# Performance work log

Measured on AMD Instinct MI355X. Metric: run time of the kernel, lower is better.

Reference implementation:

```python
import jax, jax.numpy as jnp
import numpy as np

N_NODES = 100000


def setup_inputs() -> dict:
    key = jax.random.key(0)
    k1, k2, k3, k4, k5 = jax.random.split(key, 5)
    h = jax.random.normal(k1, (N_NODES, 128), dtype=jnp.float32)
    norm = jax.random.uniform(k2, (N_NODES, 1), dtype=jnp.float32)  # D^{-1/2}-style per-node norm
    W = jax.random.normal(k3, (128, 64), dtype=jnp.float32) * 0.05
    b = jnp.zeros((64,), dtype=jnp.float32)
    src = jax.random.randint(k4, (1600000,), 0, N_NODES, dtype=jnp.int32)
    dst = jax.random.randint(k5, (1600000,), 0, N_NODES, dtype=jnp.int32)
    return {"h": h, "norm": norm, "W": W, "b": b, "src": src, "dst": dst}


def reference(h, norm, W, b, src, dst):
    # Dense feature transform: g.ndata['h'] = h @ W   (dropout is identity at inference)
    hw = jnp.matmul(h, W)  # [N, out]
    # Message: src feature scaled by src norm
    msg = hw[src] * norm[src]  # [E, out]
    # Reduce: sum messages into dst, scale by dst norm
    agg = jax.ops.segment_sum(msg, dst, num_segments=N_NODES) * norm  # [N, out]
    out = agg + b
    return jax.nn.relu(out)
```

## Files before the change

kernel.cpp:

```cpp
#include <hip/hip_runtime.h>


typedef unsigned int u32;
typedef unsigned short u16;
typedef __attribute__((ext_vector_type(8))) short s16x8;
typedef __attribute__((ext_vector_type(4))) float f32x4;

#define NB_LOG 6
#define NPB 64
#define CAP 2048
#define MAXB 2048
#define EPB 8192
#define RT 256

__device__ __forceinline__ float bf2f(u16 v) {
  return __uint_as_float(((u32)v) << 16);
}
__device__ __forceinline__ u16 f2bf(float f) {
  u32 u = __float_as_uint(f);
  return (u16)((u + 0x7fffu + ((u >> 16) & 1u)) >> 16);
}

__global__ __launch_bounds__(256) void wconv(
    const float* __restrict__ W, u16* __restrict__ Wtg, u32* __restrict__ gcur) {
  int o = blockIdx.x * 256 + threadIdx.x;
  int j = o & 7, col = (o >> 3) & 15, kq = (o >> 7) & 3, ks = (o >> 9) & 3,
      ct = (o >> 11) & 3;
  int k = ks * 32 + kq * 8 + j;
  int n = ct * 16 + col;
  Wtg[o] = f2bf(W[k * 64 + n]);
  if (o < MAXB) gcur[o] = 0;
}

__global__ __launch_bounds__(256) void gemm_mfma(
    const float* __restrict__ h, const float* __restrict__ norm,
    const u16* __restrict__ Wtg, u16* __restrict__ scaledh, int N) {
  int lane = threadIdx.x & 63, wid = threadIdx.x >> 6;
  int col = lane & 15, kq = lane >> 4;

  s16x8 bfrag[4][4];
#pragma unroll
  for (int ct = 0; ct < 4; ++ct)
#pragma unroll
    for (int ks = 0; ks < 4; ++ks) {
      int f = ct * 16 + ks * 4 + kq;
      bfrag[ct][ks] = *reinterpret_cast<const s16x8*>(Wtg + ((size_t)(f * 16 + col) * 8));
    }

  int row0 = blockIdx.x * 64 + wid * 16;
  int myrow = row0 + col;
  int ldrow = myrow < N ? myrow : (N - 1);
  const float* __restrict__ hrow = h + (size_t)ldrow * 128 + kq * 8;

  f32x4 acc[4];
#pragma unroll
  for (int ct = 0; ct < 4; ++ct) acc[ct] = (f32x4){0.f, 0.f, 0.f, 0.f};

#pragma unroll
  for (int ks = 0; ks < 4; ++ks) {
    float4 x0 = *reinterpret_cast<const float4*>(hrow + ks * 32);
    float4 x1 = *reinterpret_cast<const float4*>(hrow + ks * 32 + 4);
    s16x8 a;
    a[0] = (short)f2bf(x0.x); a[1] = (short)f2bf(x0.y);
    a[2] = (short)f2bf(x0.z); a[3] = (short)f2bf(x0.w);
    a[4] = (short)f2bf(x1.x); a[5] = (short)f2bf(x1.y);
    a[6] = (short)f2bf(x1.z); a[7] = (short)f2bf(x1.w);
#pragma unroll
    for (int ct = 0; ct < 4; ++ct)
      acc[ct] = __builtin_amdgcn_mfma_f32_16x16x32_bf16(a, bfrag[ct][ks], acc[ct], 0, 0, 0);
  }

#pragma unroll
  for (int reg = 0; reg < 4; ++reg) {
    int node = row0 + kq * 4 + reg;
    if (node < N) {
      float nm = norm[node];
#pragma unroll
      for (int ct = 0; ct < 4; ++ct)
        scaledh[(size_t)node * 64 + ct * 16 + col] = f2bf(acc[ct][reg] * nm);
    }
  }
}

__global__ __launch_bounds__(1024) void bin_edges(
    const int* __restrict__ src, const int* __restrict__ dst,
    u32* __restrict__ gcur, u32* __restrict__ bins, int E) {
  __shared__ u32 lhist[MAXB];
  __shared__ u32 lbase[MAXB];
  int t = threadIdx.x;
  for (int i = t; i < MAXB; i += 1024) lhist[i] = 0;
  __syncthreads();
  int e0 = blockIdx.x * EPB;
  int s[8], d[8];
  u32 r[8];
#pragma unroll
  for (int k = 0; k < 8; ++k) {
    int e = e0 + k * 1024 + t;
    bool ok = e < E;
    s[k] = ok ? src[e] : 0;
    d[k] = ok ? dst[e] : -1;
  }
#pragma unroll
  for (int k = 0; k < 8; ++k) {
    if (d[k] >= 0) r[k] = atomicAdd(&lhist[d[k] >> NB_LOG], 1u);
  }
  __syncthreads();
  for (int i = t; i < MAXB; i += 1024) {
    u32 c = lhist[i];
    lbase[i] = c ? atomicAdd(&gcur[i], c) : 0u;
  }
  __syncthreads();
#pragma unroll
  for (int k = 0; k < 8; ++k) {
    if (d[k] >= 0) {
      int bk = d[k] >> NB_LOG;
      u32 p = lbase[bk] + r[k];
      if (p < CAP)
        bins[(size_t)bk * CAP + p] = ((u32)s[k] << NB_LOG) | (u32)(d[k] & (NPB - 1));
    }
  }
}

__global__ __launch_bounds__(RT) void bucket_reduce(
    const u16* __restrict__ scaledh, const u32* __restrict__ bins,
    const u32* __restrict__ gcur, const float* __restrict__ norm,
    const float4* __restrict__ bias4, float* __restrict__ out, int N) {
  __shared__ u32 hist[NPB];
  __shared__ u32 startp[NPB + 1];
  __shared__ u32 sorted[CAP];
  int bkt = blockIdx.x;
  int t = threadIdx.x, lane = t & 63, wid = t >> 6;
  int cnt = (int)gcur[bkt];
  if (cnt > CAP) cnt = CAP;
  if (t < NPB) hist[t] = 0;
  __syncthreads();

  const u32* __restrict__ my = bins + (size_t)bkt * CAP;
  u32 w[CAP / RT];
  u32 rk[CAP / RT];
#pragma unroll
  for (int k = 0; k < CAP / RT; ++k) {
    int e = k * RT + t;
    w[k] = (e < cnt) ? my[e] : 0xFFFFFFFFu;
  }
#pragma unroll
  for (int k = 0; k < CAP / RT; ++k) {
    if (w[k] != 0xFFFFFFFFu)
      rk[k] = atomicAdd(&hist[w[k] & (NPB - 1)], 1u);
  }
  __syncthreads();
  if (t < NPB) {
    u32 v = hist[t];
    u32 inc = v;
#pragma unroll
    for (int m = 1; m < NPB; m <<= 1) {
      u32 x = __shfl_up(inc, m);
      if (t >= m) inc += x;
    }
    startp[t] = inc - v;
    if (t == NPB - 1) startp[NPB] = inc;
  }
  __syncthreads();
#pragma unroll
  for (int k = 0; k < CAP / RT; ++k) {
    if (w[k] != 0xFFFFFFFFu)
      sorted[startp[w[k] & (NPB - 1)] + rk[k]] = w[k] >> NB_LOG;
  }
  __syncthreads();

  int grp = lane >> 4, c4 = lane & 15;
  float4 bl = bias4[c4];
  int base = bkt << NB_LOG;
  for (int rr = wid; rr < NPB; rr += 8) {
    int rA = rr, rB = rr + 4;
    int nodeA = base + rA, nodeB = base + rB;
    int jA = (int)startp[rA] + grp, endA = (int)startp[rA + 1];
    int jB = (int)startp[rB] + grp, endB = (int)startp[rB + 1];
    float4 aA = make_float4(0.f, 0.f, 0.f, 0.f);
    float4 aB = make_float4(0.f, 0.f, 0.f, 0.f);
    while (jA < endA || jB < endB) {
      if (jA < endA) {
        int s = (int)sorted[jA];
        uint2 v = *reinterpret_cast<const uint2*>(scaledh + (size_t)s * 64 + c4 * 4);
        aA.x += __uint_as_float(v.x << 16);
        aA.y += __uint_as_float(v.x & 0xFFFF0000u);
        aA.z += __uint_as_float(v.y << 16);
        aA.w += __uint_as_float(v.y & 0xFFFF0000u);
        jA += 4;
      }
      if (jB < endB) {
        int s = (int)sorted[jB];
        uint2 v = *reinterpret_cast<const uint2*>(scaledh + (size_t)s * 64 + c4 * 4);
        aB.x += __uint_as_float(v.x << 16);
        aB.y += __uint_as_float(v.x & 0xFFFF0000u);
        aB.z += __uint_as_float(v.y << 16);
        aB.w += __uint_as_float(v.y & 0xFFFF0000u);
        jB += 4;
      }
    }
#pragma unroll
    for (int m = 16; m <= 32; m <<= 1) {
      aA.x += __shfl_xor(aA.x, m); aA.y += __shfl_xor(aA.y, m);
      aA.z += __shfl_xor(aA.z, m); aA.w += __shfl_xor(aA.w, m);
      aB.x += __shfl_xor(aB.x, m); aB.y += __shfl_xor(aB.y, m);
      aB.z += __shfl_xor(aB.z, m); aB.w += __shfl_xor(aB.w, m);
    }
    if (grp == 0) {
      if (nodeA < N) {
        float nm = norm[nodeA];
        float4 o;
        o.x = fmaxf(fmaf(aA.x, nm, bl.x), 0.f);
        o.y = fmaxf(fmaf(aA.y, nm, bl.y), 0.f);
        o.z = fmaxf(fmaf(aA.z, nm, bl.z), 0.f);
        o.w = fmaxf(fmaf(aA.w, nm, bl.w), 0.f);
        *reinterpret_cast<float4*>(out + (size_t)nodeA * 64 + c4 * 4) = o;
      }
      if (nodeB < N) {
        float nm = norm[nodeB];
        float4 o;
        o.x = fmaxf(fmaf(aB.x, nm, bl.x), 0.f);
        o.y = fmaxf(fmaf(aB.y, nm, bl.y), 0.f);
        o.z = fmaxf(fmaf(aB.z, nm, bl.z), 0.f);
        o.w = fmaxf(fmaf(aB.w, nm, bl.w), 0.f);
        *reinterpret_cast<float4*>(out + (size_t)nodeB * 64 + c4 * 4) = o;
      }
    }
  }
}

__global__ __launch_bounds__(256) void zero_out(float4* __restrict__ o4, size_t n4) {
  size_t tid = blockIdx.x * 256 + threadIdx.x;
  size_t stride = (size_t)gridDim.x * 256;
  for (size_t i = tid; i < n4; i += stride) o4[i] = make_float4(0.f, 0.f, 0.f, 0.f);
}

__global__ __launch_bounds__(256) void scatter_edges(
    const u16* __restrict__ scaledh, const int* __restrict__ src,
    const int* __restrict__ dst, float* __restrict__ agg, int E) {
  int lane = threadIdx.x & 63;
  int gwid = (blockIdx.x * 256 + threadIdx.x) >> 6;
  int nw = (gridDim.x * 256) >> 6;
  for (int e = gwid; e < E; e += nw) {
    int s = __builtin_amdgcn_readfirstlane(src[e]);
    int d = __builtin_amdgcn_readfirstlane(dst[e]);
    float v = bf2f(scaledh[(size_t)s * 64 + lane]);
    unsafeAtomicAdd(&agg[(size_t)d * 64 + lane], v);
  }
}

__global__ __launch_bounds__(256) void finalize(
    float4* __restrict__ out4, const float* __restrict__ norm,
    const float4* __restrict__ b4, int N) {
  size_t total4 = (size_t)N * 16;
  size_t tid = blockIdx.x * 256 + threadIdx.x;
  size_t stride = (size_t)gridDim.x * 256;
  for (size_t t = tid; t < total4; t += stride) {
    int i = (int)(t >> 4), q = (int)(t & 15);
    float4 v = out4[t];
    float nm = norm[i];
    float4 bb = b4[q];
    v.x = fmaxf(fmaf(v.x, nm, bb.x), 0.f);
    v.y = fmaxf(fmaf(v.y, nm, bb.y), 0.f);
    v.z = fmaxf(fmaf(v.z, nm, bb.z), 0.f);
    v.w = fmaxf(fmaf(v.w, nm, bb.w), 0.f);
    out4[t] = v;
  }
}

extern "C" void kernel_launch(void* const* d_in, const int* in_sizes, int n_in,
                              void* d_out, int out_size, void* d_ws, size_t ws_size,
                              hipStream_t stream) {
  const float* h    = (const float*)d_in[0];
  const float* norm = (const float*)d_in[1];
  const float* W    = (const float*)d_in[2];
  const float* b    = (const float*)d_in[3];
  const int*   src  = (const int*)d_in[4];
  const int*   dst  = (const int*)d_in[5];

  int N = in_sizes[1];
  int E = in_sizes[4];
  int nbuckets = (N + NPB - 1) >> NB_LOG;
  int nrb = (N + 63) >> 6;

  char* ws = (char*)d_ws;
  size_t off = 0;
  u16* scaledh = (u16*)(ws + off); off += (((size_t)N * 64 * 2) + 255) & ~(size_t)255;
  u32* gcur    = (u32*)(ws + off); off += (MAXB * 4 + 255) & ~(size_t)255;
  u16* Wtg     = (u16*)(ws + off); off += (8192 * 2 + 255) & ~(size_t)255;
  u32* bins    = (u32*)(ws + off); off += (size_t)MAXB * CAP * 4;
  size_t needed = off;
  size_t needed_fb = (size_t)((char*)bins - ws);

  if (ws_size >= needed && nbuckets <= MAXB) {
    wconv<<<32, 256, 0, stream>>>(W, Wtg, gcur);
    gemm_mfma<<<nrb, 256, 0, stream>>>(h, norm, Wtg, scaledh, N);
    bin_edges<<<(E + EPB - 1) / EPB, 1024, 0, stream>>>(src, dst, gcur, bins, E);
    bucket_reduce<<<nbuckets, RT, 0, stream>>>(scaledh, bins, gcur, norm,
                                               (const float4*)b, (float*)d_out, N);
  } else if (ws_size >= needed_fb) {
    float* agg = (float*)d_out;
    wconv<<<32, 256, 0, stream>>>(W, Wtg, gcur);
    gemm_mfma<<<nrb, 256, 0, stream>>>(h, norm, Wtg, scaledh, N);
    zero_out<<<1024, 256, 0, stream>>>((float4*)agg, (size_t)N * 16);
    scatter_edges<<<2048, 256, 0, stream>>>(scaledh, src, dst, agg, E);
    finalize<<<1024, 256, 0, stream>>>((float4*)agg, norm, (const float4*)b, N);
  }
}
```

Before: 88.28 us.

## Fuse GEMM and edge binning into one launch; restructure bucket reduce gather

```diff
diff --git a/kernel.cpp b/kernel.cpp
--- a/kernel.cpp
+++ b/kernel.cpp
@@ -19,6 +19,12 @@
 __device__ __forceinline__ u16 f2bf(float f) {
   u32 u = __float_as_uint(f);
   return (u16)((u + 0x7fffu + ((u >> 16) & 1u)) >> 16);
+}
+__device__ __forceinline__ void acc_bf16x4(float4& a, uint2 v) {
+  a.x += __uint_as_float(v.x << 16);
+  a.y += __uint_as_float(v.x & 0xFFFF0000u);
+  a.z += __uint_as_float(v.y << 16);
+  a.w += __uint_as_float(v.y & 0xFFFF0000u);
 }
 
 __global__ __launch_bounds__(256) void wconv(
@@ -32,91 +38,92 @@
   if (o < MAXB) gcur[o] = 0;
 }
 
-__global__ __launch_bounds__(256) void gemm_mfma(
+__global__ __launch_bounds__(256) void gemm_and_bin(
     const float* __restrict__ h, const float* __restrict__ norm,
-    const u16* __restrict__ Wtg, u16* __restrict__ scaledh, int N) {
-  int lane = threadIdx.x & 63, wid = threadIdx.x >> 6;
-  int col = lane & 15, kq = lane >> 4;
-
-  s16x8 bfrag[4][4];
-#pragma unroll
-  for (int ct = 0; ct < 4; ++ct)
-#pragma unroll
-    for (int ks = 0; ks < 4; ++ks) {
-      int f = ct * 16 + ks * 4 + kq;
-      bfrag[ct][ks] = *reinterpret_cast<const s16x8*>(Wtg + ((size_t)(f * 16 + col) * 8));
-    }
-
-  int row0 = blockIdx.x * 64 + wid * 16;
-  int myrow = row0 + col;
-  int ldrow = myrow < N ? myrow : (N - 1);
-  const float* __restrict__ hrow = h + (size_t)ldrow * 128 + kq * 8;
-
-  f32x4 acc[4];
-#pragma unroll
-  for (int ct = 0; ct < 4; ++ct) acc[ct] = (f32x4){0.f, 0.f, 0.f, 0.f};
-
-#pragma unroll
-  for (int ks = 0; ks < 4; ++ks) {
-    float4 x0 = *reinterpret_cast<const float4*>(hrow + ks * 32);
-    float4 x1 = *reinterpret_cast<const float4*>(hrow + ks * 32 + 4);
-    s16x8 a;
-    a[0] = (short)f2bf(x0.x); a[1] = (short)f2bf(x0.y);
-    a[2] = (short)f2bf(x0.z); a[3] = (short)f2bf(x0.w);
-    a[4] = (short)f2bf(x1.x); a[5] = (short)f2bf(x1.y);
-    a[6] = (short)f2bf(x1.z); a[7] = (short)f2bf(x1.w);
-#pragma unroll
-    for (int ct = 0; ct < 4; ++ct)
-      acc[ct] = __builtin_amdgcn_mfma_f32_16x16x32_bf16(a, bfrag[ct][ks], acc[ct], 0, 0, 0);
-  }
-
-#pragma unroll
-  for (int reg = 0; reg < 4; ++reg) {
-    int node = row0 + kq * 4 + reg;
-    if (node < N) {
-      float nm = norm[node];
-#pragma unroll
-      for (int ct = 0; ct < 4; ++ct)
-        scaledh[(size_t)node * 64 + ct * 16 + col] = f2bf(acc[ct][reg] * nm);
-    }
-  }
-}
-
-__global__ __launch_bounds__(1024) void bin_edges(
+    const u16* __restrict__ Wtg, u16* __restrict__ scaledh, int N, int nrb,
     const int* __restrict__ src, const int* __restrict__ dst,
     u32* __restrict__ gcur, u32* __restrict__ bins, int E) {
-  __shared__ u32 lhist[MAXB];
+  __shared__ u32 hist[MAXB];
   __shared__ u32 lbase[MAXB];
+
+  if ((int)blockIdx.x < nrb) {
+    int lane = threadIdx.x & 63, wid = threadIdx.x >> 6;
+    int col = lane & 15, kq = lane >> 4;
+
+    s16x8 bfrag[4][4];
+#pragma unroll
+    for (int ct = 0; ct < 4; ++ct)
+#pragma unroll
+      for (int ks = 0; ks < 4; ++ks) {
+        int f = ct * 16 + ks * 4 + kq;
+        bfrag[ct][ks] =
+            *reinterpret_cast<const s16x8*>(Wtg + ((size_t)(f * 16 + col) * 8));
+      }
+
+    int row0 = blockIdx.x * 64 + wid * 16;
+    int myrow = row0 + col;
+    int ldrow = myrow < N ? myrow : (N - 1);
+    const float* __restrict__ hrow = h + (size_t)ldrow * 128 + kq * 8;
+
+    f32x4 acc[4];
+#pragma unroll
+    for (int ct = 0; ct < 4; ++ct) acc[ct] = (f32x4){0.f, 0.f, 0.f, 0.f};
+
+#pragma unroll
+    for (int ks = 0; ks < 4; ++ks) {
+      float4 x0 = *reinterpret_cast<const float4*>(hrow + ks * 32);
+      float4 x1 = *reinterpret_cast<const float4*>(hrow + ks * 32 + 4);
+      s16x8 a;
+      a[0] = (short)f2bf(x0.x); a[1] = (short)f2bf(x0.y);
+      a[2] = (short)f2bf(x0.z); a[3] = (short)f2bf(x0.w);
+      a[4] = (short)f2bf(x1.x); a[5] = (short)f2bf(x1.y);
+      a[6] = (short)f2bf(x1.z); a[7] = (short)f2bf(x1.w);
+#pragma unroll
+      for (int ct = 0; ct < 4; ++ct)
+        acc[ct] =
+            __builtin_amdgcn_mfma_f32_16x16x32_bf16(a, bfrag[ct][ks], acc[ct], 0, 0, 0);
+    }
+
+#pragma unroll
+    for (int reg = 0; reg < 4; ++reg) {
+      int node = row0 + kq * 4 + reg;
+      if (node < N) {
+        float nm = norm[node];
+#pragma unroll
+        for (int ct = 0; ct < 4; ++ct)
+          scaledh[(size_t)node * 64 + ct * 16 + col] = f2bf(acc[ct][reg] * nm);
+      }
+    }
+    return;
+  }
+
+  int bid = (int)blockIdx.x - nrb;
   int t = threadIdx.x;
-  for (int i = t; i < MAXB; i += 1024) lhist[i] = 0;
-  __syncthreads();
-  int e0 = blockIdx.x * EPB;
-  int s[8], d[8];
-  u32 r[8];
-#pragma unroll
-  for (int k = 0; k < 8; ++k) {
-    int e = e0 + k * 1024 + t;
-    bool ok = e < E;
-    s[k] = ok ? src[e] : 0;
-    d[k] = ok ? dst[e] : -1;
-  }
-#pragma unroll
-  for (int k = 0; k < 8; ++k) {
-    if (d[k] >= 0) r[k] = atomicAdd(&lhist[d[k] >> NB_LOG], 1u);
-  }
-  __syncthreads();
-  for (int i = t; i < MAXB; i += 1024) {
-    u32 c = lhist[i];
+  for (int i = t; i < MAXB; i += 256) hist[i] = 0;
+  __syncthreads();
+  int e0 = bid * EPB;
+#pragma unroll 4
+  for (int k = 0; k < EPB / 256; ++k) {
+    int e = e0 + k * 256 + t;
+    if (e < E) atomicAdd(&hist[dst[e] >> NB_LOG], 1u);
+  }
+  __syncthreads();
+  for (int i = t; i < MAXB; i += 256) {
+    u32 c = hist[i];
     lbase[i] = c ? atomicAdd(&gcur[i], c) : 0u;
   }
   __syncthreads();
-#pragma unroll
-  for (int k = 0; k < 8; ++k) {
-    if (d[k] >= 0) {
-      int bk = d[k] >> NB_LOG;
-      u32 p = lbase[bk] + r[k];
+  for (int i = t; i < MAXB; i += 256) hist[i] = 0;
+  __syncthreads();
+#pragma unroll 4
+  for (int k = 0; k < EPB / 256; ++k) {
+    int e = e0 + k * 256 + t;
+    if (e < E) {
+      int d = dst[e], s = src[e];
+      int bk = d >> NB_LOG;
+      u32 p = lbase[bk] + atomicAdd(&hist[bk], 1u);
       if (p < CAP)
-        bins[(size_t)bk * CAP + p] = ((u32)s[k] << NB_LOG) | (u32)(d[k] & (NPB - 1));
+        bins[(size_t)bk * CAP + p] = ((u32)s << NB_LOG) | (u32)(d & (NPB - 1));
     }
   }
 }
@@ -171,59 +178,54 @@
   int grp = lane >> 4, c4 = lane & 15;
   float4 bl = bias4[c4];
   int base = bkt << NB_LOG;
-  for (int rr = wid; rr < NPB; rr += 8) {
-    int rA = rr, rB = rr + 4;
-    int nodeA = base + rA, nodeB = base + rB;
-    int jA = (int)startp[rA] + grp, endA = (int)startp[rA + 1];
-    int jB = (int)startp[rB] + grp, endB = (int)startp[rB + 1];
+  int cm1 = cnt - 1;
+#pragma unroll
+  for (int round = 0; round < 2; ++round) {
+    int rA = (wid << 4) + (round << 3) + grp;
+    int rB = rA + 4;
+    int jA = (int)startp[rA], eA = (int)startp[rA + 1];
+    int jB = (int)startp[rB], eB = (int)startp[rB + 1];
     float4 aA = make_float4(0.f, 0.f, 0.f, 0.f);
     float4 aB = make_float4(0.f, 0.f, 0.f, 0.f);
-    while (jA < endA || jB < endB) {
-      if (jA < endA) {
-        int s = (int)sorted[jA];
-        uint2 v = *reinterpret_cast<const uint2*>(scaledh + (size_t)s * 64 + c4 * 4);
-        aA.x += __uint_as_float(v.x << 16);
-        aA.y += __uint_as_float(v.x & 0xFFFF0000u);
-        aA.z += __uint_as_float(v.y << 16);
-        aA.w += __uint_as_float(v.y & 0xFFFF0000u);
-        jA += 4;
-      }
-      if (jB < endB) {
-        int s = (int)sorted[jB];
-        uint2 v = *reinterpret_cast<const uint2*>(scaledh + (size_t)s * 64 + c4 * 4);
-        aB.x += __uint_as_float(v.x << 16);
-        aB.y += __uint_as_float(v.x & 0xFFFF0000u);
-        aB.z += __uint_as_float(v.y << 16);
-        aB.w += __uint_as_float(v.y & 0xFFFF0000u);
-        jB += 4;
-      }
-    }
-#pragma unroll
-    for (int m = 16; m <= 32; m <<= 1) {
-      aA.x += __shfl_xor(aA.x, m); aA.y += __shfl_xor(aA.y, m);
-      aA.z += __shfl_xor(aA.z, m); aA.w += __shfl_xor(aA.w, m);
-      aB.x += __shfl_xor(aB.x, m); aB.y += __shfl_xor(aB.y, m);
-      aB.z += __shfl_xor(aB.z, m); aB.w += __shfl_xor(aB.w, m);
-    }
-    if (grp == 0) {
-      if (nodeA < N) {
-        float nm = norm[nodeA];
-        float4 o;
-        o.x = fmaxf(fmaf(aA.x, nm, bl.x), 0.f);
-        o.y = fmaxf(fmaf(aA.y, nm, bl.y), 0.f);
-        o.z = fmaxf(fmaf(aA.z, nm, bl.z), 0.f);
-        o.w = fmaxf(fmaf(aA.w, nm, bl.w), 0.f);
-        *reinterpret_cast<float4*>(out + (size_t)nodeA * 64 + c4 * 4) = o;
-      }
-      if (nodeB < N) {
-        float nm = norm[nodeB];
-        float4 o;
-        o.x = fmaxf(fmaf(aB.x, nm, bl.x), 0.f);
-        o.y = fmaxf(fmaf(aB.y, nm, bl.y), 0.f);
-        o.z = fmaxf(fmaf(aB.z, nm, bl.z), 0.f);
-        o.w = fmaxf(fmaf(aB.w, nm, bl.w), 0.f);
-        *reinterpret_cast<float4*>(out + (size_t)nodeB * 64 + c4 * 4) = o;
-      }
+    while (jA < eA || jB < eB) {
+      int iA0 = (int)sorted[min(jA, cm1)];
+      int iA1 = (int)sorted[min(jA + 1, cm1)];
+      int iB0 = (int)sorted[min(jB, cm1)];
+      int iB1 = (int)sorted[min(jB + 1, cm1)];
+      uint2 vA0 = *reinterpret_cast<const uint2*>(scaledh + ((size_t)iA0 << 6) + (c4 << 2));
+      uint2 vA1 = *reinterpret_cast<const uint2*>(scaledh + ((size_t)iA1 << 6) + (c4 << 2));
+      uint2 vB0 = *reinterpret_cast<const uint2*>(scaledh + ((size_t)iB0 << 6) + (c4 << 2));
+      uint2 vB1 = *reinterpret_cast<const uint2*>(scaledh + ((size_t)iB1 << 6) + (c4 << 2));
+      uint2 z = make_uint2(0u, 0u);
+      vA0 = (jA < eA) ? vA0 : z;
+      vA1 = (jA + 1 < eA) ? vA1 : z;
+      vB0 = (jB < eB) ? vB0 : z;
+      vB1 = (jB + 1 < eB) ? vB1 : z;
+      acc_bf16x4(aA, vA0);
+      acc_bf16x4(aA, vA1);
+      acc_bf16x4(aB, vB0);
+      acc_bf16x4(aB, vB1);
+      jA += 2;
+      jB += 2;
+    }
+    int nodeA = base + rA, nodeB = base + rB;
+    if (nodeA < N) {
+      float nm = norm[nodeA];
+      float4 o;
+      o.x = fmaxf(fmaf(aA.x, nm, bl.x), 0.f);
+      o.y = fmaxf(fmaf(aA.y, nm, bl.y), 0.f);
+      o.z = fmaxf(fmaf(aA.z, nm, bl.z), 0.f);
+      o.w = fmaxf(fmaf(aA.w, nm, bl.w), 0.f);
+      *reinterpret_cast<float4*>(out + (size_t)nodeA * 64 + (c4 << 2)) = o;
+    }
+    if (nodeB < N) {
+      float nm = norm[nodeB];
+      float4 o;
+      o.x = fmaxf(fmaf(aB.x, nm, bl.x), 0.f);
+      o.y = fmaxf(fmaf(aB.y, nm, bl.y), 0.f);
+      o.z = fmaxf(fmaf(aB.z, nm, bl.z), 0.f);
+      o.w = fmaxf(fmaf(aB.w, nm, bl.w), 0.f);
+      *reinterpret_cast<float4*>(out + (size_t)nodeB * 64 + (c4 << 2)) = o;
     }
   }
 }
@@ -281,6 +283,7 @@
   int E = in_sizes[4];
   int nbuckets = (N + NPB - 1) >> NB_LOG;
   int nrb = (N + 63) >> 6;
+  int nbinb = (E + EPB - 1) / EPB;
 
   char* ws = (char*)d_ws;
   size_t off = 0;
@@ -293,14 +296,15 @@
 
   if (ws_size >= needed && nbuckets <= MAXB) {
     wconv<<<32, 256, 0, stream>>>(W, Wtg, gcur);
-    gemm_mfma<<<nrb, 256, 0, stream>>>(h, norm, Wtg, scaledh, N);
-    bin_edges<<<(E + EPB - 1) / EPB, 1024, 0, stream>>>(src, dst, gcur, bins, E);
+    gemm_and_bin<<<nrb + nbinb, 256, 0, stream>>>(h, norm, Wtg, scaledh, N, nrb,
+                                                  src, dst, gcur, bins, E);
     bucket_reduce<<<nbuckets, RT, 0, stream>>>(scaledh, bins, gcur, norm,
                                                (const float4*)b, (float*)d_out, N);
   } else if (ws_size >= needed_fb) {
     float* agg = (float*)d_out;
     wconv<<<32, 256, 0, stream>>>(W, Wtg, gcur);
-    gemm_mfma<<<nrb, 256, 0, stream>>>(h, norm, Wtg, scaledh, N);
+    gemm_and_bin<<<nrb, 256, 0, stream>>>(h, norm, Wtg, scaledh, N, nrb,
+                                          src, dst, gcur, bins, E);
     zero_out<<<1024, 256, 0, stream>>>((float4*)agg, (size_t)N * 16);
     scatter_edges<<<2048, 256, 0, stream>>>(scaledh, src, dst, agg, E);
     finalize<<<1024, 256, 0, stream>>>((float4*)agg, norm, (const float4*)b, N);
```

After: 93.29 us. 5.7% more time.
